# Performance work log

Hardware: AMD Instinct MI355X
Metric: run time of the kernel (lower is better)

## Reference

```python
import jax, jax.numpy as jnp
import numpy as np

B, V, FN, C = 8, 50000, 100000, 64


def setup_inputs() -> dict:
    key = jax.random.key(0)
    keys = iter(jax.random.split(key, 16))
    inp = {}
    inp["centers"] = jax.random.normal(next(keys), (B, 3, FN), jnp.float32)
    inp["verts"] = jax.random.normal(next(keys), (B, V, 3), jnp.float32)
    inp["faces"] = jax.random.randint(next(keys), (B, FN, 3), 0, V)

    def bn(p):
        inp[p + "g"] = jnp.ones((C,), jnp.float32)
        inp[p + "bt"] = jnp.zeros((C,), jnp.float32)
        inp[p + "m"] = jnp.zeros((C,), jnp.float32)
        inp[p + "v"] = jnp.ones((C,), jnp.float32)

    inp["cw1"] = jax.random.normal(next(keys), (C, 3), jnp.float32) * 0.1
    inp["cb1"] = jnp.zeros((C,), jnp.float32); bn("c1")
    inp["cw2"] = jax.random.normal(next(keys), (C, C), jnp.float32) * 0.1
    inp["cb2"] = jnp.zeros((C,), jnp.float32); bn("c2")
    inp["vw1"] = jax.random.normal(next(keys), (C, 6), jnp.float32) * 0.1
    inp["vb1"] = jnp.zeros((C,), jnp.float32); bn("v1")
    inp["vw2"] = jax.random.normal(next(keys), (C, C), jnp.float32) * 0.1
    inp["vb2"] = jnp.zeros((C,), jnp.float32); bn("v2")
    inp["sw"] = jax.random.normal(next(keys), (C, 2 * C), jnp.float32) * 0.1
    inp["sb"] = jnp.zeros((C,), jnp.float32); bn("s1")
    return inp


def _cbr(x, w, b, g, bt, m, v, eps=1e-5):
    # 1x1 Conv1d == pointwise GEMM over channel dim, then eval-mode BN, then ReLU
    y = jnp.einsum('bcf,oc->bof', x, w) + b[:, None]
    y = (y - m[:, None]) * (g[:, None] / jnp.sqrt(v[:, None] + eps)) + bt[:, None]
    return jax.nn.relu(y)


def _forward(faces, centers, verts,
             cw1, cb1, c1g, c1bt, c1m, c1v, cw2, cb2, c2g, c2bt, c2m, c2v,
             vw1, vb1, v1g, v1bt, v1m, v1v, vw2, vb2, v2g, v2bt, v2m, v2v,
             sw, sb, s1g, s1bt, s1m, s1v):
    Bb, Fn, _ = faces.shape
    # gather 3 corner vertices per face: [B, 3F, 3] -> [B, 9, F] (v0xyz, v1xyz, v2xyz)
    idx = faces.reshape(Bb, Fn * 3)
    corners = jnp.take_along_axis(verts, idx[:, :, None], axis=1)
    c9 = corners.reshape(Bb, Fn, 9).transpose(0, 2, 1)

    def vmlp(x):
        return _cbr(_cbr(x, vw1, vb1, v1g, v1bt, v1m, v1v), vw2, vb2, v2g, v2bt, v2m, v2v)

    vfeat = (vmlp(c9[:, :6])
             + vmlp(c9[:, 3:9])
             + vmlp(jnp.concatenate([c9[:, 6:9], c9[:, :3]], axis=1))) / 3.0
    cfeat = _cbr(_cbr(centers, cw1, cb1, c1g, c1bt, c1m, c1v), cw2, cb2, c2g, c2bt, c2m, c2v)
    return _cbr(jnp.concatenate([cfeat, vfeat], axis=1), sw, sb, s1g, s1bt, s1m, s1v)


def reference(centers, verts, faces,
              cw1, cb1, c1g, c1bt, c1m, c1v, cw2, cb2, c2g, c2bt, c2m, c2v,
              vw1, vb1, v1g, v1bt, v1m, v1v, vw2, vb2, v2g, v2bt, v2m, v2v,
              sw, sb, s1g, s1bt, s1m, s1v):
    return _forward(faces, centers, verts,
                    cw1, cb1, c1g, c1bt, c1m, c1v, cw2, cb2, c2g, c2bt, c2m, c2v,
                    vw1, vb1, v1g, v1bt, v1m, v1v, vw2, vb2, v2g, v2bt, v2m, v2v,
                    sw, sb, s1g, s1bt, s1m, s1v)
```

## Files before the change

kernel.cpp:

```cpp
#include <hip/hip_runtime.h>
#include <cstddef>
#include <cstdint>

#define FN_ 100000
#define V_  50000
#define B_  8
#define NT  128
#define NBX 782

#define WS_SHS 49152

typedef _Float16 f16;
typedef f16   f16x8 __attribute__((ext_vector_type(8)));
typedef float f32x4 __attribute__((ext_vector_type(4)));

struct Ptrs { const void* p[33]; };

union Pk4 { f16 h[4]; uint2 u; };
union Pk8 { f16 h[8]; uint4 u; };

__global__ __launch_bounds__(1024) void sd_prep(Ptrs in, f16* __restrict__ wsW,
                                                float* __restrict__ shsG)
{
  const float* __restrict__ cw1 = (const float*)in.p[3];
  const float* __restrict__ cb1 = (const float*)in.p[4];
  const float* __restrict__ c1g = (const float*)in.p[5];
  const float* __restrict__ c1bt= (const float*)in.p[6];
  const float* __restrict__ c1m = (const float*)in.p[7];
  const float* __restrict__ c1v = (const float*)in.p[8];
  const float* __restrict__ cw2 = (const float*)in.p[9];
  const float* __restrict__ cb2 = (const float*)in.p[10];
  const float* __restrict__ c2g = (const float*)in.p[11];
  const float* __restrict__ c2bt= (const float*)in.p[12];
  const float* __restrict__ c2m = (const float*)in.p[13];
  const float* __restrict__ c2v = (const float*)in.p[14];
  const float* __restrict__ vw1 = (const float*)in.p[15];
  const float* __restrict__ vb1 = (const float*)in.p[16];
  const float* __restrict__ v1g = (const float*)in.p[17];
  const float* __restrict__ v1bt= (const float*)in.p[18];
  const float* __restrict__ v1m = (const float*)in.p[19];
  const float* __restrict__ v1v = (const float*)in.p[20];
  const float* __restrict__ vw2 = (const float*)in.p[21];
  const float* __restrict__ vb2 = (const float*)in.p[22];
  const float* __restrict__ v2g = (const float*)in.p[23];
  const float* __restrict__ v2bt= (const float*)in.p[24];
  const float* __restrict__ v2m = (const float*)in.p[25];
  const float* __restrict__ v2v = (const float*)in.p[26];
  const float* __restrict__ sw  = (const float*)in.p[27];
  const float* __restrict__ sb  = (const float*)in.p[28];
  const float* __restrict__ s1g = (const float*)in.p[29];
  const float* __restrict__ s1bt= (const float*)in.p[30];
  const float* __restrict__ s1m = (const float*)in.p[31];
  const float* __restrict__ s1v = (const float*)in.p[32];

  __shared__ float scsL[448];
  const int tid = threadIdx.x;

  if (tid < 448) {
    const float *g, *v, *bb, *m, *bt; int o; float mul = 1.f;
    if (tid < 64)       { o = tid;      g=c1g; v=c1v; bb=cb1; m=c1m; bt=c1bt; }
    else if (tid < 256) { o = tid & 63; g=v1g; v=v1v; bb=vb1; m=v1m; bt=v1bt; }
    else if (tid < 320) { o = tid-256;  g=c2g; v=c2v; bb=cb2; m=c2m; bt=c2bt; }
    else if (tid < 384) { o = tid-320;  g=v2g; v=v2v; bb=vb2; m=v2m; bt=v2bt; mul = 1.f/3.f; }
    else                { o = tid-384;  g=s1g; v=s1v; bb=sb;  m=s1m; bt=s1bt; }
    float s = g[o] * rsqrtf(v[o] + 1e-5f);
    scsL[tid] = s * mul;
    shsG[tid] = ((bb[o] - m[o]) * s + bt[o]) * mul;
  }
  __syncthreads();

  for (int u = tid; u < 3072; u += 1024) {
    const int t = u >> 6, l = u & 63, r15 = l & 15, g4 = l >> 4;
    Pk8 pk;
    if (t < 16) {
      const int wm = t >> 2, tr = t & 3, row = 64*wm + 16*tr + r15;
#pragma unroll
      for (int j = 0; j < 8; ++j) {
        const int k = 8*g4 + j; float val = 0.f;
        if (wm == 0) { if (k >= 9 && k < 12) val = cw1[row*3 + (k-9)]; }
        else if (k < 9) {
          const int e = wm - 1, o = row - 64*wm, c = (k - 3*e + 9) % 9;
          if (c < 6) val = vw1[o*6 + c];
        }
        pk.h[j] = (f16)(val * scsL[row]);
      }
    } else if (t < 24) {
      const int tt = t-16, rt = tt >> 1, s = tt & 1, row = 16*rt + r15;
#pragma unroll
      for (int j = 0; j < 8; ++j) { const int k = 32*s + 8*g4 + j;
        pk.h[j] = (f16)(cw2[row*64 + k] * scsL[256+row]); }
    } else if (t < 32) {
      const int tt = t-24, rt = tt >> 1, s = tt & 1, row = 16*rt + r15;
#pragma unroll
      for (int j = 0; j < 8; ++j) { const int k = 32*s + 8*g4 + j;
        pk.h[j] = (f16)(vw2[row*64 + k] * scsL[320+row]); }
    } else {
      const int tt = t-32, rt = tt >> 2, s = tt & 3, row = 16*rt + r15;
#pragma unroll
      for (int j = 0; j < 8; ++j) { const int k = 32*s + 8*g4 + j;
        pk.h[j] = (f16)(sw[row*128 + k] * scsL[384+row]); }
    }
    *(uint4*)(wsW + (size_t)t*512 + l*8) = pk.u;
  }
}

__global__ __launch_bounds__(512, 6) void sd_main(const int* __restrict__ faces,
    const float* __restrict__ verts, const float* __restrict__ centers,
    const f16* __restrict__ wsW, const float* __restrict__ shsG,
    float* __restrict__ out)
{
  __shared__ f16 Hs[NT][168];
  __shared__ float shsL[448];

  const int tid  = threadIdx.x;
  const int lane = tid & 63;
  const int r15  = lane & 15;
  const int g4   = lane >> 4;
  const int wid  = __builtin_amdgcn_readfirstlane(tid >> 6);
  const int rt   = wid & 3;
  const int cg   = wid >> 2;

  const int by   = blockIdx.y;
  const int col0 = blockIdx.x * NT;

  if (tid < 448) shsL[tid] = shsG[tid];

  {
    const int col = tid >> 2, p = tid & 3;
    const int f = col0 + col;
    const bool valid = f < FN_;
    if (p < 3) {
      float x0 = 0.f, x1 = 0.f, x2 = 0.f;
      if (valid) {
        const int vi = faces[((size_t)by*FN_ + f)*3 + p];
        const float* vp = verts + ((size_t)by*V_ + (size_t)vi)*3;
        x0 = vp[0]; x1 = vp[1]; x2 = vp[2];
      }
      Hs[col][128 + p*3 + 0] = (f16)x0;
      Hs[col][128 + p*3 + 1] = (f16)x1;
      Hs[col][128 + p*3 + 2] = (f16)x2;
    } else {
#pragma unroll
      for (int k = 0; k < 3; ++k)
        Hs[col][137 + k] = valid ? (f16)centers[((size_t)by*3 + k)*FN_ + f] : (f16)0.f;
    }
#pragma unroll
    for (int z = 0; z < 5; ++z) Hs[col][140 + p*5 + z] = (f16)0.f;
  }
  __syncthreads();

  float cf[4][4], vf[4][4];
  f16x8 w2v[2];

#pragma unroll
  for (int h = 0; h < 2; ++h) {
    {
      f16x8 bfr[4];
#pragma unroll
      for (int tc = 0; tc < 4; ++tc)
        bfr[tc] = *(const f16x8*)&Hs[64*cg + 16*tc + r15][128 + 8*g4];
#pragma unroll
      for (int tr = 0; tr < 2; ++tr) {
        const int t16 = 2*rt + tr;
        const f16x8 a = *(const f16x8*)(wsW + (size_t)(8*h + t16)*512 + lane*8);
        const f32x4 shv = *(const f32x4*)&shsL[128*h + t16*16 + 4*g4];
#pragma unroll
        for (int tc = 0; tc < 4; ++tc) {
          f32x4 acc = shv;
          acc = __builtin_amdgcn_mfma_f32_16x16x32_f16(a, bfr[tc], acc, 0,0,0);
          Pk4 pk;
#pragma unroll
          for (int j = 0; j < 4; ++j) pk.h[j] = (f16)fmaxf(acc[j], 0.f);
          *(uint2*)&Hs[64*cg + 16*tc + r15][t16*16 + 4*g4] = pk.u;
        }
      }
    }
    __syncthreads();

#pragma unroll
    for (int sub = 0; sub < 2; ++sub) {
      const bool is_cf = (h == 0) && (sub == 0);
      f16x8 wa[2];
      if (is_cf) {
#pragma unroll
        for (int s = 0; s < 2; ++s)
          wa[s] = *(const f16x8*)(wsW + (size_t)(16 + 2*rt + s)*512 + lane*8);
      } else if (h == 0) {
#pragma unroll
        for (int s = 0; s < 2; ++s) {
          w2v[s] = *(const f16x8*)(wsW + (size_t)(24 + 2*rt + s)*512 + lane*8);
          wa[s] = w2v[s];
        }
      } else {
#pragma unroll
        for (int s = 0; s < 2; ++s) wa[s] = w2v[s];
      }
      const f32x4 shv = is_cf ? *(const f32x4*)&shsL[256 + rt*16 + 4*g4]
                              : *(const f32x4*)&shsL[320 + rt*16 + 4*g4];
      f32x4 acc[4];
#pragma unroll
      for (int tc = 0; tc < 4; ++tc) acc[tc] = shv;
#pragma unroll
      for (int s = 0; s < 2; ++s) {
#pragma unroll
        for (int tc = 0; tc < 4; ++tc) {
          const f16x8 b = *(const f16x8*)&Hs[64*cg + 16*tc + r15][64*sub + 32*s + 8*g4];
          acc[tc] = __builtin_amdgcn_mfma_f32_16x16x32_f16(wa[s], b, acc[tc], 0,0,0);
        }
      }
#pragma unroll
      for (int tc = 0; tc < 4; ++tc)
#pragma unroll
        for (int j = 0; j < 4; ++j) {
          const float val = fmaxf(acc[tc][j], 0.f);
          if (is_cf)       cf[tc][j]  = val;
          else if (h == 0 && sub == 1) vf[tc][j]  = val;
          else             vf[tc][j] += val;
        }
    }
    __syncthreads();
  }

#pragma unroll
  for (int tc = 0; tc < 4; ++tc) {
    const int o0  = rt*16 + 4*g4;
    const int col = 64*cg + 16*tc + r15;
    Pk4 pc, pv;
#pragma unroll
    for (int j = 0; j < 4; ++j) { pc.h[j] = (f16)cf[tc][j]; pv.h[j] = (f16)vf[tc][j]; }
    *(uint2*)&Hs[col][o0]      = pc.u;
    *(uint2*)&Hs[col][64 + o0] = pv.u;
  }
  __syncthreads();

  {
    const f32x4 shv = *(const f32x4*)&shsL[384 + rt*16 + 4*g4];
    f32x4 acc[4];
#pragma unroll
    for (int tc = 0; tc < 4; ++tc) acc[tc] = shv;
#pragma unroll
    for (int s = 0; s < 4; ++s) {
      const f16x8 a = *(const f16x8*)(wsW + (size_t)(32 + rt*4 + s)*512 + lane*8);
#pragma unroll
      for (int tc = 0; tc < 4; ++tc) {
        const f16x8 b = *(const f16x8*)&Hs[64*cg + 16*tc + r15][32*s + 8*g4];
        acc[tc] = __builtin_amdgcn_mfma_f32_16x16x32_f16(a, b, acc[tc], 0,0,0);
      }
    }
    const int o0 = rt*16 + 4*g4;
#pragma unroll
    for (int tc = 0; tc < 4; ++tc) {
      const int f = col0 + 64*cg + 16*tc + r15;
      if (f < FN_) {
        const size_t base = ((size_t)(by*64 + o0))*FN_ + f;
#pragma unroll
        for (int j = 0; j < 4; ++j)
          out[base + (size_t)j*FN_] = fmaxf(acc[tc][j], 0.f);
      }
    }
  }
}

extern "C" void kernel_launch(void* const* d_in, const int* in_sizes, int n_in,
                              void* d_out, int out_size, void* d_ws, size_t ws_size,
                              hipStream_t stream) {
  (void)in_sizes; (void)n_in; (void)out_size; (void)ws_size;
  Ptrs p;
  for (int i = 0; i < 33; ++i) p.p[i] = d_in[i];
  f16*   wsW  = (f16*)d_ws;
  float* shsG = (float*)((char*)d_ws + WS_SHS);
  hipLaunchKernelGGL(sd_prep, dim3(1), dim3(1024), 0, stream, p, wsW, shsG);
  hipLaunchKernelGGL(sd_main, dim3(NBX, B_), dim3(512), 0, stream,
                     (const int*)d_in[2], (const float*)d_in[1], (const float*)d_in[0],
                     wsW, shsG, (float*)d_out);
}
```

Measured before the change: 104.8 us.

## Give each wave its own 32-column tile with LDS-staged weights, dropping block barriers

Each wave now owns 32 face columns end to end and computes all 64 output rows, so intermediate activations live in per-wave LDS slices and the inner __syncthreads calls go away. All fp16 weights are copied once per block into LDS instead of being read from global memory per MFMA. The gather is reworked to two threads per face with packed stores, and the block tile grows to 256 columns. In exchange, LDS use rises to roughly 120KB per block and occupancy drops (launch bounds 6 to 2), and each wave now holds more accumulator registers.

```diff
diff --git a/kernel.cpp b/kernel.cpp
--- a/kernel.cpp
+++ b/kernel.cpp
@@ -5,8 +5,8 @@
 #define FN_ 100000
 #define V_  50000
 #define B_  8
-#define NT  128
-#define NBX 782
+#define NT  256
+#define NBX ((FN_ + NT - 1) / NT)
 
 #define WS_SHS 49152
 
@@ -16,6 +16,7 @@
 
 struct Ptrs { const void* p[33]; };
 
+union Pk2 { f16 h[2]; uint32_t u; };
 union Pk4 { f16 h[4]; uint2 u; };
 union Pk8 { f16 h[8]; uint4 u; };
 
@@ -104,158 +105,168 @@
   }
 }
 
-__global__ __launch_bounds__(512, 6) void sd_main(const int* __restrict__ faces,
+__global__ __launch_bounds__(512, 2) void sd_main(const int* __restrict__ faces,
     const float* __restrict__ verts, const float* __restrict__ centers,
     const f16* __restrict__ wsW, const float* __restrict__ shsG,
     float* __restrict__ out)
 {
-  __shared__ f16 Hs[NT][168];
+  __shared__ f16 Wl[24576];
+  __shared__ f16 Hb[8][32][136];
+  __shared__ f16 Xb[8][32][40];
   __shared__ float shsL[448];
 
   const int tid  = threadIdx.x;
   const int lane = tid & 63;
   const int r15  = lane & 15;
   const int g4   = lane >> 4;
-  const int wid  = __builtin_amdgcn_readfirstlane(tid >> 6);
-  const int rt   = wid & 3;
-  const int cg   = wid >> 2;
-
+  const int w    = __builtin_amdgcn_readfirstlane(tid >> 6);
   const int by   = blockIdx.y;
   const int col0 = blockIdx.x * NT;
 
+  {
+    const uint4* src = (const uint4*)wsW;
+    uint4* dst = (uint4*)Wl;
+#pragma unroll
+    for (int i = 0; i < 6; ++i) dst[tid + i*512] = src[tid + i*512];
+  }
   if (tid < 448) shsL[tid] = shsG[tid];
 
   {
-    const int col = tid >> 2, p = tid & 3;
+    const int col = tid >> 1, p = tid & 1;
+    const int wg = col >> 5, cl = col & 31;
     const int f = col0 + col;
     const bool valid = f < FN_;
-    if (p < 3) {
-      float x0 = 0.f, x1 = 0.f, x2 = 0.f;
-      if (valid) {
-        const int vi = faces[((size_t)by*FN_ + f)*3 + p];
-        const float* vp = verts + ((size_t)by*V_ + (size_t)vi)*3;
-        x0 = vp[0]; x1 = vp[1]; x2 = vp[2];
-      }
-      Hs[col][128 + p*3 + 0] = (f16)x0;
-      Hs[col][128 + p*3 + 1] = (f16)x1;
-      Hs[col][128 + p*3 + 2] = (f16)x2;
+    const size_t fb3 = ((size_t)by*FN_ + (size_t)(valid ? f : 0)) * 3;
+    f16* xrow = &Xb[wg][cl][0];
+    if (p == 0) {
+      const int i0 = faces[fb3 + 0], i1 = faces[fb3 + 1];
+      const float* q0 = verts + ((size_t)by*V_ + (size_t)i0)*3;
+      const float* q1 = verts + ((size_t)by*V_ + (size_t)i1)*3;
+      float v0=0.f,v1=0.f,v2=0.f,v3=0.f,v4=0.f,v5=0.f;
+      if (valid) { v0=q0[0]; v1=q0[1]; v2=q0[2]; v3=q1[0]; v4=q1[1]; v5=q1[2]; }
+      Pk2 a,b,c;
+      a.h[0]=(f16)v0; a.h[1]=(f16)v1; b.h[0]=(f16)v2; b.h[1]=(f16)v3;
+      c.h[0]=(f16)v4; c.h[1]=(f16)v5;
+      *(uint32_t*)&xrow[0] = a.u; *(uint32_t*)&xrow[2] = b.u; *(uint32_t*)&xrow[4] = c.u;
+#pragma unroll
+      for (int z = 0; z < 5; ++z) *(uint32_t*)&xrow[12 + 2*z] = 0u;
     } else {
-#pragma unroll
-      for (int k = 0; k < 3; ++k)
-        Hs[col][137 + k] = valid ? (f16)centers[((size_t)by*3 + k)*FN_ + f] : (f16)0.f;
-    }
-#pragma unroll
-    for (int z = 0; z < 5; ++z) Hs[col][140 + p*5 + z] = (f16)0.f;
+      const int i2 = faces[fb3 + 2];
+      const float* q2 = verts + ((size_t)by*V_ + (size_t)i2)*3;
+      float v0=0.f,v1=0.f,v2=0.f,v3=0.f,v4=0.f,v5=0.f;
+      if (valid) { v0=q2[0]; v1=q2[1]; v2=q2[2];
+                   v3=centers[((size_t)by*3+0)*FN_ + f];
+                   v4=centers[((size_t)by*3+1)*FN_ + f];
+                   v5=centers[((size_t)by*3+2)*FN_ + f]; }
+      Pk2 a,b,c;
+      a.h[0]=(f16)v0; a.h[1]=(f16)v1; b.h[0]=(f16)v2; b.h[1]=(f16)v3;
+      c.h[0]=(f16)v4; c.h[1]=(f16)v5;
+      *(uint32_t*)&xrow[6] = a.u; *(uint32_t*)&xrow[8] = b.u; *(uint32_t*)&xrow[10] = c.u;
+#pragma unroll
+      for (int z = 0; z < 5; ++z) *(uint32_t*)&xrow[22 + 2*z] = 0u;
+    }
   }
   __syncthreads();
 
-  float cf[4][4], vf[4][4];
-  f16x8 w2v[2];
+  const f16x8 bx0 = *(const f16x8*)&Xb[w][r15][8*g4];
+  const f16x8 bx1 = *(const f16x8*)&Xb[w][16 + r15][8*g4];
+
+  float cf[4][2][4], vf[4][2][4];
 
 #pragma unroll
   for (int h = 0; h < 2; ++h) {
-    {
-      f16x8 bfr[4];
-#pragma unroll
-      for (int tc = 0; tc < 4; ++tc)
-        bfr[tc] = *(const f16x8*)&Hs[64*cg + 16*tc + r15][128 + 8*g4];
-#pragma unroll
-      for (int tr = 0; tr < 2; ++tr) {
-        const int t16 = 2*rt + tr;
-        const f16x8 a = *(const f16x8*)(wsW + (size_t)(8*h + t16)*512 + lane*8);
-        const f32x4 shv = *(const f32x4*)&shsL[128*h + t16*16 + 4*g4];
-#pragma unroll
-        for (int tc = 0; tc < 4; ++tc) {
-          f32x4 acc = shv;
-          acc = __builtin_amdgcn_mfma_f32_16x16x32_f16(a, bfr[tc], acc, 0,0,0);
-          Pk4 pk;
-#pragma unroll
-          for (int j = 0; j < 4; ++j) pk.h[j] = (f16)fmaxf(acc[j], 0.f);
-          *(uint2*)&Hs[64*cg + 16*tc + r15][t16*16 + 4*g4] = pk.u;
+#pragma unroll
+    for (int t = 0; t < 8; ++t) {
+      const int tg = 8*h + t;
+      const f16x8 a = *(const f16x8*)&Wl[tg*512 + lane*8];
+      const f32x4 shv = *(const f32x4*)&shsL[tg*16 + 4*g4];
+      f32x4 a0 = __builtin_amdgcn_mfma_f32_16x16x32_f16(a, bx0, shv, 0,0,0);
+      f32x4 a1 = __builtin_amdgcn_mfma_f32_16x16x32_f16(a, bx1, shv, 0,0,0);
+      Pk4 p0, p1;
+#pragma unroll
+      for (int j = 0; j < 4; ++j) {
+        p0.h[j] = (f16)fmaxf(a0[j], 0.f);
+        p1.h[j] = (f16)fmaxf(a1[j], 0.f);
+      }
+      *(uint2*)&Hb[w][r15][t*16 + 4*g4]      = p0.u;
+      *(uint2*)&Hb[w][16 + r15][t*16 + 4*g4] = p1.u;
+    }
+
+#pragma unroll
+    for (int sub = 0; sub < 2; ++sub) {
+      const bool is_c = (h == 0 && sub == 0);
+      const int wbase = is_c ? 16 : 24;
+      const int shb   = is_c ? 256 : 320;
+      f16x8 Bf[2][2];
+#pragma unroll
+      for (int cg = 0; cg < 2; ++cg)
+#pragma unroll
+        for (int s = 0; s < 2; ++s)
+          Bf[cg][s] = *(const f16x8*)&Hb[w][16*cg + r15][64*sub + 32*s + 8*g4];
+#pragma unroll
+      for (int rt = 0; rt < 4; ++rt) {
+        const f16x8 a0 = *(const f16x8*)&Wl[(wbase + 2*rt + 0)*512 + lane*8];
+        const f16x8 a1 = *(const f16x8*)&Wl[(wbase + 2*rt + 1)*512 + lane*8];
+        const f32x4 shv = *(const f32x4*)&shsL[shb + rt*16 + 4*g4];
+#pragma unroll
+        for (int cg = 0; cg < 2; ++cg) {
+          f32x4 acc = __builtin_amdgcn_mfma_f32_16x16x32_f16(a0, Bf[cg][0], shv, 0,0,0);
+          acc = __builtin_amdgcn_mfma_f32_16x16x32_f16(a1, Bf[cg][1], acc, 0,0,0);
+#pragma unroll
+          for (int j = 0; j < 4; ++j) {
+            const float val = fmaxf(acc[j], 0.f);
+            if (h == 0) { if (sub == 0) cf[rt][cg][j] = val; else vf[rt][cg][j] = val; }
+            else        vf[rt][cg][j] += val;
+          }
         }
       }
     }
-    __syncthreads();
-
-#pragma unroll
-    for (int sub = 0; sub < 2; ++sub) {
-      const bool is_cf = (h == 0) && (sub == 0);
-      f16x8 wa[2];
-      if (is_cf) {
-#pragma unroll
-        for (int s = 0; s < 2; ++s)
-          wa[s] = *(const f16x8*)(wsW + (size_t)(16 + 2*rt + s)*512 + lane*8);
-      } else if (h == 0) {
-#pragma unroll
-        for (int s = 0; s < 2; ++s) {
-          w2v[s] = *(const f16x8*)(wsW + (size_t)(24 + 2*rt + s)*512 + lane*8);
-          wa[s] = w2v[s];
+  }
+
+#pragma unroll
+  for (int rt = 0; rt < 4; ++rt)
+#pragma unroll
+    for (int cg = 0; cg < 2; ++cg) {
+      Pk4 pc, pv;
+#pragma unroll
+      for (int j = 0; j < 4; ++j) {
+        pc.h[j] = (f16)cf[rt][cg][j];
+        pv.h[j] = (f16)vf[rt][cg][j];
+      }
+      *(uint2*)&Hb[w][16*cg + r15][rt*16 + 4*g4]      = pc.u;
+      *(uint2*)&Hb[w][16*cg + r15][64 + rt*16 + 4*g4] = pv.u;
+    }
+
+  {
+    f32x4 acc[4][2];
+#pragma unroll
+    for (int rt = 0; rt < 4; ++rt) {
+      const f32x4 shv = *(const f32x4*)&shsL[384 + rt*16 + 4*g4];
+      acc[rt][0] = shv; acc[rt][1] = shv;
+    }
+#pragma unroll
+    for (int s = 0; s < 4; ++s) {
+      const f16x8 b0 = *(const f16x8*)&Hb[w][r15][32*s + 8*g4];
+      const f16x8 b1 = *(const f16x8*)&Hb[w][16 + r15][32*s + 8*g4];
+#pragma unroll
+      for (int rt = 0; rt < 4; ++rt) {
+        const f16x8 a = *(const f16x8*)&Wl[(32 + rt*4 + s)*512 + lane*8];
+        acc[rt][0] = __builtin_amdgcn_mfma_f32_16x16x32_f16(a, b0, acc[rt][0], 0,0,0);
+        acc[rt][1] = __builtin_amdgcn_mfma_f32_16x16x32_f16(a, b1, acc[rt][1], 0,0,0);
+      }
+    }
+    const int fbase = col0 + 32*w + r15;
+#pragma unroll
+    for (int cg = 0; cg < 2; ++cg) {
+      const int f = fbase + 16*cg;
+      if (f < FN_) {
+#pragma unroll
+        for (int rt = 0; rt < 4; ++rt) {
+          const size_t base = ((size_t)(by*64 + rt*16 + 4*g4))*FN_ + (size_t)f;
+#pragma unroll
+          for (int j = 0; j < 4; ++j)
+            out[base + (size_t)j*FN_] = fmaxf(acc[rt][cg][j], 0.f);
         }
-      } else {
-#pragma unroll
-        for (int s = 0; s < 2; ++s) wa[s] = w2v[s];
-      }
-      const f32x4 shv = is_cf ? *(const f32x4*)&shsL[256 + rt*16 + 4*g4]
-                              : *(const f32x4*)&shsL[320 + rt*16 + 4*g4];
-      f32x4 acc[4];
-#pragma unroll
-      for (int tc = 0; tc < 4; ++tc) acc[tc] = shv;
-#pragma unroll
-      for (int s = 0; s < 2; ++s) {
-#pragma unroll
-        for (int tc = 0; tc < 4; ++tc) {
-          const f16x8 b = *(const f16x8*)&Hs[64*cg + 16*tc + r15][64*sub + 32*s + 8*g4];
-          acc[tc] = __builtin_amdgcn_mfma_f32_16x16x32_f16(wa[s], b, acc[tc], 0,0,0);
-        }
-      }
-#pragma unroll
-      for (int tc = 0; tc < 4; ++tc)
-#pragma unroll
-        for (int j = 0; j < 4; ++j) {
-          const float val = fmaxf(acc[tc][j], 0.f);
-          if (is_cf)       cf[tc][j]  = val;
-          else if (h == 0 && sub == 1) vf[tc][j]  = val;
-          else             vf[tc][j] += val;
-        }
-    }
-    __syncthreads();
-  }
-
-#pragma unroll
-  for (int tc = 0; tc < 4; ++tc) {
-    const int o0  = rt*16 + 4*g4;
-    const int col = 64*cg + 16*tc + r15;
-    Pk4 pc, pv;
-#pragma unroll
-    for (int j = 0; j < 4; ++j) { pc.h[j] = (f16)cf[tc][j]; pv.h[j] = (f16)vf[tc][j]; }
-    *(uint2*)&Hs[col][o0]      = pc.u;
-    *(uint2*)&Hs[col][64 + o0] = pv.u;
-  }
-  __syncthreads();
-
-  {
-    const f32x4 shv = *(const f32x4*)&shsL[384 + rt*16 + 4*g4];
-    f32x4 acc[4];
-#pragma unroll
-    for (int tc = 0; tc < 4; ++tc) acc[tc] = shv;
-#pragma unroll
-    for (int s = 0; s < 4; ++s) {
-      const f16x8 a = *(const f16x8*)(wsW + (size_t)(32 + rt*4 + s)*512 + lane*8);
-#pragma unroll
-      for (int tc = 0; tc < 4; ++tc) {
-        const f16x8 b = *(const f16x8*)&Hs[64*cg + 16*tc + r15][32*s + 8*g4];
-        acc[tc] = __builtin_amdgcn_mfma_f32_16x16x32_f16(a, b, acc[tc], 0,0,0);
-      }
-    }
-    const int o0 = rt*16 + 4*g4;
-#pragma unroll
-    for (int tc = 0; tc < 4; ++tc) {
-      const int f = col0 + 64*cg + 16*tc + r15;
-      if (f < FN_) {
-        const size_t base = ((size_t)(by*64 + o0))*FN_ + f;
-#pragma unroll
-        for (int j = 0; j < 4; ++j)
-          out[base + (size_t)j*FN_] = fmaxf(acc[tc][j], 0.f);
       }
     }
   }
```

After: 126.0 us. +20.1%, slower.

## Halve face tile, compute all first-layer outputs at once, pack ReLU in f16

Applied to the files above, without the earlier changes.

The tile shrinks from 128 to 64 faces per block, and the LDS row widens so every first-layer output (two hidden MLP inputs plus the three vertex-pair variants) is computed in one pass before a single barrier. This replaces the two-half loop with its extra syncs. Each wave now handles 2 column tiles instead of 4, and occupancy is raised to 8 blocks. ReLU+convert uses packed cvt_pkrtz plus v_pk_max_f16, which rounds toward zero rather than to nearest. The cost is twice as many blocks, each doing more redundant weight loads and setup, and fewer MFMAs per weight fragment.

```diff
diff --git a/kernel.cpp b/kernel.cpp
--- a/kernel.cpp
+++ b/kernel.cpp
@@ -5,8 +5,8 @@
 #define FN_ 100000
 #define V_  50000
 #define B_  8
-#define NT  128
-#define NBX 782
+#define NT  64
+#define NBX ((FN_ + NT - 1) / NT)
 
 #define WS_SHS 49152
 
@@ -16,8 +16,16 @@
 
 struct Ptrs { const void* p[33]; };
 
-union Pk4 { f16 h[4]; uint2 u; };
 union Pk8 { f16 h[8]; uint4 u; };
+
+__device__ __forceinline__ uint32_t pack2(float a, float b) {
+  return __builtin_bit_cast(uint32_t, __builtin_amdgcn_cvt_pkrtz(a, b));
+}
+__device__ __forceinline__ uint32_t pack_relu2(float a, float b) {
+  uint32_t r, x = pack2(a, b);
+  asm("v_pk_max_f16 %0, %1, 0" : "=v"(r) : "v"(x));
+  return r;
+}
 
 __global__ __launch_bounds__(1024) void sd_prep(Ptrs in, f16* __restrict__ wsW,
                                                 float* __restrict__ shsG)
@@ -104,29 +112,26 @@
   }
 }
 
-__global__ __launch_bounds__(512, 6) void sd_main(const int* __restrict__ faces,
+__global__ __launch_bounds__(512, 8) void sd_main(const int* __restrict__ faces,
     const float* __restrict__ verts, const float* __restrict__ centers,
     const f16* __restrict__ wsW, const float* __restrict__ shsG,
     float* __restrict__ out)
 {
-  __shared__ f16 Hs[NT][168];
+  __shared__ f16 Hs[NT][296];
   __shared__ float shsL[448];
 
   const int tid  = threadIdx.x;
   const int lane = tid & 63;
   const int r15  = lane & 15;
   const int g4   = lane >> 4;
-  const int wid  = __builtin_amdgcn_readfirstlane(tid >> 6);
-  const int rt   = wid & 3;
-  const int cg   = wid >> 2;
-
+  const int w    = __builtin_amdgcn_readfirstlane(tid >> 6);
   const int by   = blockIdx.y;
   const int col0 = blockIdx.x * NT;
 
   if (tid < 448) shsL[tid] = shsG[tid];
 
   {
-    const int col = tid >> 2, p = tid & 3;
+    const int col = tid >> 3, p = tid & 7;
     const int f = col0 + col;
     const bool valid = f < FN_;
     if (p < 3) {
@@ -136,123 +141,100 @@
         const float* vp = verts + ((size_t)by*V_ + (size_t)vi)*3;
         x0 = vp[0]; x1 = vp[1]; x2 = vp[2];
       }
-      Hs[col][128 + p*3 + 0] = (f16)x0;
-      Hs[col][128 + p*3 + 1] = (f16)x1;
-      Hs[col][128 + p*3 + 2] = (f16)x2;
+      Hs[col][256 + p*3 + 0] = (f16)x0;
+      Hs[col][256 + p*3 + 1] = (f16)x1;
+      Hs[col][256 + p*3 + 2] = (f16)x2;
+    } else if (p == 3) {
+#pragma unroll
+      for (int k = 0; k < 3; ++k)
+        Hs[col][265 + k] = valid ? (f16)centers[((size_t)by*3 + k)*FN_ + f] : (f16)0.f;
     } else {
 #pragma unroll
-      for (int k = 0; k < 3; ++k)
-        Hs[col][137 + k] = valid ? (f16)centers[((size_t)by*3 + k)*FN_ + f] : (f16)0.f;
-    }
-#pragma unroll
-    for (int z = 0; z < 5; ++z) Hs[col][140 + p*5 + z] = (f16)0.f;
-  }
-  __syncthreads();
-
-  float cf[4][4], vf[4][4];
-  f16x8 w2v[2];
-
-#pragma unroll
-  for (int h = 0; h < 2; ++h) {
-    {
-      f16x8 bfr[4];
-#pragma unroll
-      for (int tc = 0; tc < 4; ++tc)
-        bfr[tc] = *(const f16x8*)&Hs[64*cg + 16*tc + r15][128 + 8*g4];
-#pragma unroll
-      for (int tr = 0; tr < 2; ++tr) {
-        const int t16 = 2*rt + tr;
-        const f16x8 a = *(const f16x8*)(wsW + (size_t)(8*h + t16)*512 + lane*8);
-        const f32x4 shv = *(const f32x4*)&shsL[128*h + t16*16 + 4*g4];
-#pragma unroll
-        for (int tc = 0; tc < 4; ++tc) {
-          f32x4 acc = shv;
-          acc = __builtin_amdgcn_mfma_f32_16x16x32_f16(a, bfr[tc], acc, 0,0,0);
-          Pk4 pk;
-#pragma unroll
-          for (int j = 0; j < 4; ++j) pk.h[j] = (f16)fmaxf(acc[j], 0.f);
-          *(uint2*)&Hs[64*cg + 16*tc + r15][t16*16 + 4*g4] = pk.u;
-        }
-      }
-    }
-    __syncthreads();
-
-#pragma unroll
-    for (int sub = 0; sub < 2; ++sub) {
-      const bool is_cf = (h == 0) && (sub == 0);
-      f16x8 wa[2];
-      if (is_cf) {
-#pragma unroll
-        for (int s = 0; s < 2; ++s)
-          wa[s] = *(const f16x8*)(wsW + (size_t)(16 + 2*rt + s)*512 + lane*8);
-      } else if (h == 0) {
-#pragma unroll
-        for (int s = 0; s < 2; ++s) {
-          w2v[s] = *(const f16x8*)(wsW + (size_t)(24 + 2*rt + s)*512 + lane*8);
-          wa[s] = w2v[s];
-        }
-      } else {
-#pragma unroll
-        for (int s = 0; s < 2; ++s) wa[s] = w2v[s];
-      }
-      const f32x4 shv = is_cf ? *(const f32x4*)&shsL[256 + rt*16 + 4*g4]
-                              : *(const f32x4*)&shsL[320 + rt*16 + 4*g4];
-      f32x4 acc[4];
-#pragma unroll
-      for (int tc = 0; tc < 4; ++tc) acc[tc] = shv;
-#pragma unroll
-      for (int s = 0; s < 2; ++s) {
-#pragma unroll
-        for (int tc = 0; tc < 4; ++tc) {
-          const f16x8 b = *(const f16x8*)&Hs[64*cg + 16*tc + r15][64*sub + 32*s + 8*g4];
-          acc[tc] = __builtin_amdgcn_mfma_f32_16x16x32_f16(wa[s], b, acc[tc], 0,0,0);
-        }
-      }
-#pragma unroll
-      for (int tc = 0; tc < 4; ++tc)
-#pragma unroll
-        for (int j = 0; j < 4; ++j) {
-          const float val = fmaxf(acc[tc][j], 0.f);
-          if (is_cf)       cf[tc][j]  = val;
-          else if (h == 0 && sub == 1) vf[tc][j]  = val;
-          else             vf[tc][j] += val;
-        }
-    }
-    __syncthreads();
-  }
-
-#pragma unroll
-  for (int tc = 0; tc < 4; ++tc) {
+      for (int z = 0; z < 5; ++z) Hs[col][268 + (p-4)*5 + z] = (f16)0.f;
+    }
+  }
+  __syncthreads();
+
+  const f16* __restrict__ wfrag = wsW + lane*8;
+
+  {
+    const int t0 = 2*w, t1 = 2*w + 1;
+    const f16x8 a0 = *(const f16x8*)(wfrag + (size_t)t0*512);
+    const f16x8 a1 = *(const f16x8*)(wfrag + (size_t)t1*512);
+    const f32x4 sh0 = *(const f32x4*)&shsL[t0*16 + 4*g4];
+    const f32x4 sh1 = *(const f32x4*)&shsL[t1*16 + 4*g4];
+#pragma unroll
+    for (int tc = 0; tc < 4; ++tc) {
+      const f16x8 b = *(const f16x8*)&Hs[16*tc + r15][256 + 8*g4];
+      f32x4 c0 = __builtin_amdgcn_mfma_f32_16x16x32_f16(a0, b, sh0, 0,0,0);
+      f32x4 c1 = __builtin_amdgcn_mfma_f32_16x16x32_f16(a1, b, sh1, 0,0,0);
+      uint2 p0, p1;
+      p0.x = pack_relu2(c0[0], c0[1]); p0.y = pack_relu2(c0[2], c0[3]);
+      p1.x = pack_relu2(c1[0], c1[1]); p1.y = pack_relu2(c1[2], c1[3]);
+      *(uint2*)&Hs[16*tc + r15][t0*16 + 4*g4] = p0;
+      *(uint2*)&Hs[16*tc + r15][t1*16 + 4*g4] = p1;
+    }
+  }
+  __syncthreads();
+
+  const int rt = w & 3, cg = w >> 2;
+  float cf[2][4], vf[2][4];
+
+#pragma unroll
+  for (int br = 0; br < 4; ++br) {
+    const int wbase = br ? 24 : 16;
+    const f16x8 a0 = *(const f16x8*)(wfrag + (size_t)(wbase + 2*rt + 0)*512);
+    const f16x8 a1 = *(const f16x8*)(wfrag + (size_t)(wbase + 2*rt + 1)*512);
+    const f32x4 shv = *(const f32x4*)&shsL[(br ? 320 : 256) + rt*16 + 4*g4];
+#pragma unroll
+    for (int tc = 0; tc < 2; ++tc) {
+      const int col = 16*(2*cg + tc) + r15;
+      const f16x8 b0 = *(const f16x8*)&Hs[col][64*br + 8*g4];
+      const f16x8 b1 = *(const f16x8*)&Hs[col][64*br + 32 + 8*g4];
+      f32x4 acc = __builtin_amdgcn_mfma_f32_16x16x32_f16(a0, b0, shv, 0,0,0);
+      acc = __builtin_amdgcn_mfma_f32_16x16x32_f16(a1, b1, acc, 0,0,0);
+#pragma unroll
+      for (int j = 0; j < 4; ++j) {
+        const float val = fmaxf(acc[j], 0.f);
+        if (br == 0)      cf[tc][j]  = val;
+        else if (br == 1) vf[tc][j]  = val;
+        else              vf[tc][j] += val;
+      }
+    }
+  }
+  __syncthreads();
+
+#pragma unroll
+  for (int tc = 0; tc < 2; ++tc) {
+    const int col = 16*(2*cg + tc) + r15;
     const int o0  = rt*16 + 4*g4;
-    const int col = 64*cg + 16*tc + r15;
-    Pk4 pc, pv;
-#pragma unroll
-    for (int j = 0; j < 4; ++j) { pc.h[j] = (f16)cf[tc][j]; pv.h[j] = (f16)vf[tc][j]; }
-    *(uint2*)&Hs[col][o0]      = pc.u;
-    *(uint2*)&Hs[col][64 + o0] = pv.u;
+    uint2 pc, pv;
+    pc.x = pack2(cf[tc][0], cf[tc][1]); pc.y = pack2(cf[tc][2], cf[tc][3]);
+    pv.x = pack2(vf[tc][0], vf[tc][1]); pv.y = pack2(vf[tc][2], vf[tc][3]);
+    *(uint2*)&Hs[col][o0]      = pc;
+    *(uint2*)&Hs[col][64 + o0] = pv;
   }
   __syncthreads();
 
   {
     const f32x4 shv = *(const f32x4*)&shsL[384 + rt*16 + 4*g4];
-    f32x4 acc[4];
-#pragma unroll
-    for (int tc = 0; tc < 4; ++tc) acc[tc] = shv;
+    f32x4 acc[2];
+    acc[0] = shv; acc[1] = shv;
 #pragma unroll
     for (int s = 0; s < 4; ++s) {
-      const f16x8 a = *(const f16x8*)(wsW + (size_t)(32 + rt*4 + s)*512 + lane*8);
-#pragma unroll
-      for (int tc = 0; tc < 4; ++tc) {
-        const f16x8 b = *(const f16x8*)&Hs[64*cg + 16*tc + r15][32*s + 8*g4];
+      const f16x8 a = *(const f16x8*)(wfrag + (size_t)(32 + rt*4 + s)*512);
+#pragma unroll
+      for (int tc = 0; tc < 2; ++tc) {
+        const f16x8 b = *(const f16x8*)&Hs[16*(2*cg + tc) + r15][32*s + 8*g4];
         acc[tc] = __builtin_amdgcn_mfma_f32_16x16x32_f16(a, b, acc[tc], 0,0,0);
       }
     }
     const int o0 = rt*16 + 4*g4;
 #pragma unroll
-    for (int tc = 0; tc < 4; ++tc) {
-      const int f = col0 + 64*cg + 16*tc + r15;
+    for (int tc = 0; tc < 2; ++tc) {
+      const int f = col0 + 16*(2*cg + tc) + r15;
       if (f < FN_) {
-        const size_t base = ((size_t)(by*64 + o0))*FN_ + f;
+        const size_t base = ((size_t)(by*64 + o0))*FN_ + (size_t)f;
 #pragma unroll
         for (int j = 0; j < 4; ++j)
           out[base + (size_t)j*FN_] = fmaxf(acc[tc][j], 0.f);
```

New measurement: 100.5 us. 4.2% less time.
